# Optimization experiments

Measured on AMD Instinct MI355X. Metric: run time of the kernel, lower is better.

Reference implementation:

```python
import jax, jax.numpy as jnp
import numpy as np

N, B, E, H, Z, L = 8192, 256, 163840, 128, 256, 4
NFREQ = 10
EDGE_IN = 2 * H + 9 + 2 * NFREQ * 3  # 325


def _sin_emb(x):
    # SinusoidsEmbedding: x (E,3) -> (E, 2*NFREQ*3)
    freqs = 2 * jnp.pi * jnp.arange(NFREQ, dtype=x.dtype)
    e = (x[..., None] * freqs).reshape(x.shape[0], -1)  # (E, 3*NFREQ)
    return jnp.concatenate([jnp.sin(e), jnp.cos(e)], axis=-1)


def _seg_mean(x, idx, n):
    s = jax.ops.segment_sum(x, idx, num_segments=n)
    c = jax.ops.segment_sum(jnp.ones((x.shape[0], 1), x.dtype), idx, num_segments=n)
    return s / jnp.maximum(c, 1.0)  # empty segments -> 0, matching torch scatter-mean


def setup_inputs() -> dict:
    key = jax.random.key(0)
    ks = jax.random.split(key, 20)
    atom_types = jax.random.randint(ks[0], (N,), 0, 100)
    frac_coords = jax.random.uniform(ks[1], (N, 3), dtype=jnp.float32)
    lattices = jax.random.normal(ks[2], (B, 3, 3), dtype=jnp.float32)
    z = jax.random.normal(ks[3], (B, Z), dtype=jnp.float32)
    cemb = jax.random.uniform(ks[4], (B, 1), dtype=jnp.float32)
    edge_index = jax.random.randint(ks[5], (2, E), 0, N)
    node2graph = jnp.repeat(jnp.arange(B), N // B)  # 32 atoms per graph, sorted
    w = lambda k, *s: jax.random.normal(k, s, dtype=jnp.float32) * 0.05
    z0 = lambda *s: jnp.zeros(s, jnp.float32)
    return dict(
        atom_types=atom_types, frac_coords=frac_coords, lattices=lattices,
        z=z, cemb=cemb, edge_index=edge_index, node2graph=node2graph,
        emb_table=w(ks[6], 100, H),
        W_latent=w(ks[7], H + Z, H), b_latent=z0(H),
        edge_w1=w(ks[8], L, EDGE_IN, H), edge_b1=z0(L, H),
        edge_w2=w(ks[9], L, H, H), edge_b2=z0(L, H),
        node_w1=w(ks[10], L, 2 * H, H), node_b1=z0(L, H),
        node_w2=w(ks[11], L, H, H), node_b2=z0(L, H),
        mixin_w=w(ks[12], L, H, H),
        adapt_w1=w(ks[13], L, 1, H), adapt_b1=z0(L, H),
        adapt_w2=w(ks[14], L, H, H), adapt_b2=z0(L, H),
        W_coord=w(ks[15], H, 3),
        W_lattice=w(ks[16], H, 9),
    )


def _forward(frac_coords, lattices, z, cemb, emb_table, W_latent, b_latent,
             edge_w1, edge_b1, edge_w2, edge_b2, node_w1, node_b1, node_w2, node_b2,
             mixin_w, adapt_w1, adapt_b1, adapt_w2, adapt_b2, W_coord, W_lattice,
             atom_types, edge_index, node2graph):
    silu = jax.nn.silu
    src, dst = edge_index[0], edge_index[1]
    edge2graph = node2graph[src]
    # node embedding + latent conditioning
    h = emb_table[atom_types]  # (N,H)
    h = jnp.concatenate([h, z[node2graph]], axis=-1) @ W_latent + b_latent
    # per-edge geometric features (same across layers since frac_coords fixed)
    frac_diff = (frac_coords[dst] - frac_coords[src]) % 1.0  # (E,3)
    dis = _sin_emb(frac_diff)  # (E,60)
    # ip=True: lattice inner products, flattened per graph then gathered per edge
    lat_ips = jnp.einsum('bij,bkj->bik', lattices, lattices).reshape(B, 9)
    lat_e = lat_ips[edge2graph]  # (E,9)
    n = h.shape[0]
    for i in range(L):
        hi, hj = h[src], h[dst]
        einp = jnp.concatenate([hi, hj, dis, lat_e], axis=-1)  # (E,325)
        ef = silu(silu(einp @ edge_w1[i] + edge_b1[i]) @ edge_w2[i] + edge_b2[i])
        agg = _seg_mean(ef, src, n)  # scatter-mean back to src nodes
        nout = silu(silu(jnp.concatenate([h, agg], axis=-1) @ node_w1[i] + node_b1[i])
                    @ node_w2[i] + node_b2[i])
        h = h + nout  # residual
        # conditional-embedding adapter + mixin, broadcast per-graph to nodes
        c = silu(silu(cemb @ adapt_w1[i] + adapt_b1[i]) @ adapt_w2[i] + adapt_b2[i]) @ mixin_w[i]
        h = h + c[node2graph]
    coord_out = h @ W_coord  # (N,3), no bias
    graph_f = _seg_mean(h, node2graph, B)
    lattice_out = (graph_f @ W_lattice).reshape(B, 3, 3)
    lattice_out = jnp.einsum('bij,bjk->bik', lattice_out, lattices)  # ip=True
    return lattice_out, coord_out


def reference(atom_types, frac_coords, lattices, z, cemb, edge_index, node2graph,
              emb_table, W_latent, b_latent, edge_w1, edge_b1, edge_w2, edge_b2,
              node_w1, node_b1, node_w2, node_b2, mixin_w, adapt_w1, adapt_b1,
              adapt_w2, adapt_b2, W_coord, W_lattice):
    return _forward(frac_coords, lattices, z, cemb, emb_table, W_latent, b_latent,
                    edge_w1, edge_b1, edge_w2, edge_b2, node_w1, node_b1, node_w2,
                    node_b2, mixin_w, adapt_w1, adapt_b1, adapt_w2, adapt_b2,
                    W_coord, W_lattice, atom_types, edge_index, node2graph)
```

## Files before the change

### kernel.cpp

```cpp
#include <hip/hip_runtime.h>
#include <hip/hip_bf16.h>
#include <stdint.h>

#define NN 8192
#define BB 256
#define EE 163840
#define HH 128
#define ZZ 256
#define LL 4
#define TPB 5

typedef unsigned short u16;
typedef float  f32x4  __attribute__((ext_vector_type(4)));
typedef __bf16 bf16x8 __attribute__((ext_vector_type(8)));

__device__ __forceinline__ u16 f2bf(float f) {
  union { float f; uint32_t u; } v; v.f = f;
  uint32_t r = v.u + 0x7fffu + ((v.u >> 16) & 1u);
  return (u16)(r >> 16);
}
__device__ __forceinline__ float silu_f(float x) {
  return x * __builtin_amdgcn_rcpf(1.0f + __expf(-x));
}

// ... 18 lines not shown
    __syncthreads();
  }
  const int base = (t == 0) ? 0 : part[t - 1];
#pragma unroll
  for (int j = 0; j < 8; ++j) cursor[t * 8 + j] = base + v[j];
}

__global__ void k_scatter(const int* __restrict__ ei, int* __restrict__ cursor,
                          int* __restrict__ perm) {
  const int e = blockIdx.x * 256 + threadIdx.x;
  if (e < EE) {
    const int s = ei[e];
    const int ppos = atomicAdd(&cursor[s], 1);
    perm[ppos] = e;
  }
}

#define R_WT1S  (LL * 128 * 128)
#define R_WT1D  (LL * 128 * 128)
#define R_WT1G  (LL * 128 * 64)
#define R_WT2   (LL * 128 * 128)
#define R_NWT1  (LL * 128 * 256)
#define R_NWT2  (LL * 128 * 128)
#define R_HWT   (128 * 384)
#define R_EMB   (100 * 128)
#define R_Z     (BB * ZZ)
#define R_LIP   (BB * 9)
#define PREP_TOT (R_WT1S + R_WT1D + R_WT1G + R_WT2 + R_NWT1 + R_NWT2 + R_HWT + R_EMB + R_Z + R_LIP)

__global__ __launch_bounds__(256) void k_prep(
    const float* __restrict__ ew1, const float* __restrict__ ew2,
    const float* __restrict__ nw1, const float* __restrict__ nw2,
    const float* __restrict__ Wl,  const float* __restrict__ emb,
    const float* __restrict__ z,   const float* __restrict__ lat,
    u16* __restrict__ wt1s, u16* __restrict__ wt1d, u16* __restrict__ wt1g,
    u16* __restrict__ wt2,
    u16* __restrict__ nwt1, u16* __restrict__ nwt2,
    u16* __restrict__ hwt, u16* __restrict__ embbf, u16* __restrict__ zbf,
    float* __restrict__ lip) {
  int idx = blockIdx.x * 256 + threadIdx.x;
  if (idx < R_WT1S) {
    const int l = idx >> 14, rem = idx & 16383;
    const int n = rem >> 7, k = rem & 127;
    wt1s[idx] = f2bf(ew1[((size_t)l * 325 + k) * 128 + n]);
    return;
  }
  idx -= R_WT1S;
  if (idx < R_WT1D) {
    const int l = idx >> 14, rem = idx & 16383;
    const int n = rem >> 7, k = rem & 127;
    wt1d[idx] = f2bf(ew1[((size_t)l * 325 + 128 + k) * 128 + n]);
    return;
  }
  idx -= R_WT1D;
// ... 21 lines not shown
  if (idx < R_NWT2) {
    const int l = idx >> 14, rem = idx & 16383;
    const int n = rem >> 7, k = rem & 127;
    nwt2[idx] = f2bf(nw2[((size_t)l * 128 + k) * 128 + n]);
    return;
  }
  idx -= R_NWT2;
  if (idx < R_HWT) {
    const int n = idx / 384, k = idx % 384;
    hwt[idx] = f2bf(Wl[k * 128 + n]);
    return;
  }
  idx -= R_HWT;
  if (idx < R_EMB) { embbf[idx] = f2bf(emb[idx]); return; }
  idx -= R_EMB;
  if (idx < R_Z) { zbf[idx] = f2bf(z[idx]); return; }
  idx -= R_Z;
  if (idx < R_LIP) {
    const int b = idx / 9, j = idx % 9, i = j / 3, kk = j % 3;
    float s = 0.f;
#pragma unroll
    for (int mm = 0; mm < 3; ++mm) s += lat[b * 9 + i * 3 + mm] * lat[b * 9 + kk * 3 + mm];
    lip[b * 12 + j] = s;
  }
}

__global__ void k_gl(const float* __restrict__ ew1, const float* __restrict__ eb1,
                     const float* __restrict__ lip, float* __restrict__ Gl) {
  const int idx = blockIdx.x * 256 + threadIdx.x;
  if (idx >= LL * BB * 128) return;
  const int l = idx >> 15, rem = idx & 32767, g = rem >> 7, c = rem & 127;
  float s = eb1[l * 128 + c];
#pragma unroll
  for (int j = 0; j < 9; ++j)
    s += lip[g * 12 + j] * ew1[((size_t)l * 325 + 316 + j) * 128 + c];
  Gl[idx] = s;
}

__global__ __launch_bounds__(128) void k_adapt(
    const float* __restrict__ cemb, const float* __restrict__ aw1,
    const float* __restrict__ ab1, const float* __restrict__ aw2,
    const float* __restrict__ ab2, const float* __restrict__ mixin,
    float* __restrict__ call) {
  __shared__ float s1[128], s2[128];
  const int l = blockIdx.x >> 8, b = blockIdx.x & 255, c = threadIdx.x;
  const float ce = cemb[b];
  s1[c] = silu_f(ce * aw1[l * 128 + c] + ab1[l * 128 + c]);
  __syncthreads();
  float a = ab2[l * 128 + c];
  for (int k = 0; k < 128; ++k) a += s1[k] * aw2[(l * 128 + k) * 128 + c];
  s2[c] = silu_f(a);
  __syncthreads();
  float o = 0.f;
  for (int k = 0; k < 128; ++k) o += s2[k] * mixin[(l * 128 + k) * 128 + c];
  call[((size_t)l * 256 + b) * 128 + c] = o;
}

__global__ __launch_bounds__(256) void k_h0(
    const int* __restrict__ at, const int* __restrict__ n2g,
    const u16* __restrict__ embbf, const u16* __restrict__ zbf,
    const u16* __restrict__ hwt, const float* __restrict__ bl,
    float* __restrict__ h, u16* __restrict__ hbf) {
  __shared__ __align__(16) __bf16 einp[32][392];
  const int tid = threadIdx.x, lane = tid & 63, w = tid >> 6;
  const int lr = lane & 15, lk = (lane >> 4) * 8, rr = (lane >> 4) * 4;
  const int m = tid >> 3, p = tid & 7;
  const int n0 = blockIdx.x * 32;
  {
    const int n = n0 + m;
    const uint4* er = (const uint4*)(embbf + (size_t)at[n] * 128);
    *(uint4*)(&einp[m][p * 16])     = er[p * 2];
    *(uint4*)(&einp[m][p * 16 + 8]) = er[p * 2 + 1];
    const uint4* zr = (const uint4*)(zbf + (size_t)n2g[n] * 256);
#pragma unroll
    for (int q = 0; q < 4; ++q)
      *(uint4*)(&einp[m][128 + p * 32 + q * 8]) = zr[p * 4 + q];
  }
  __syncthreads();
  f32x4 acc[2][2] = {};
  const u16* w0 = hwt + (size_t)(w * 32 + lr) * 384 + lk;
  const u16* w1 = hwt + (size_t)(w * 32 + 16 + lr) * 384 + lk;
#pragma unroll
  for (int kb = 0; kb < 12; ++kb) {
    bf16x8 a0 = *(const bf16x8*)(&einp[lr][kb * 32 + lk]);
    bf16x8 a1 = *(const bf16x8*)(&einp[16 + lr][kb * 32 + lk]);
    bf16x8 b0 = *(const bf16x8*)(w0 + kb * 32);
    bf16x8 b1 = *(const bf16x8*)(w1 + kb * 32);
    acc[0][0] = __builtin_amdgcn_mfma_f32_16x16x32_bf16(a0, b0, acc[0][0], 0, 0, 0);
    acc[0][1] = __builtin_amdgcn_mfma_f32_16x16x32_bf16(a0, b1, acc[0][1], 0, 0, 0);
    acc[1][0] = __builtin_amdgcn_mfma_f32_16x16x32_bf16(a1, b0, acc[1][0], 0, 0, 0);
    acc[1][1] = __builtin_amdgcn_mfma_f32_16x16x32_bf16(a1, b1, acc[1][1], 0, 0, 0);
  }
#pragma unroll
  for (int mt = 0; mt < 2; ++mt)
#pragma unroll
    for (int nt = 0; nt < 2; ++nt) {
      const int col = w * 32 + nt * 16 + lr;
      const float bias = bl[col];
#pragma unroll
      for (int r = 0; r < 4; ++r) {
        const int n = n0 + mt * 16 + rr + r;
        const float s = acc[mt][nt][r] + bias;
        h[(size_t)n * 128 + col] = s;
        hbf[(size_t)n * 128 + col] = f2bf(s);
      }
    }
}

__global__ __launch_bounds__(256) void k_pnode(
    const u16* __restrict__ hbf, const u16* __restrict__ wt1s,
    const u16* __restrict__ wt1d, const float* __restrict__ Gl,
    const int* __restrict__ n2g, float* __restrict__ Ps, float* __restrict__ Pd) {
  __shared__ __align__(16) __bf16 hs[32][136];
  const int tid = threadIdx.x, lane = tid & 63, w = tid >> 6;
  const int lr = lane & 15, lk = (lane >> 4) * 8, rr = (lane >> 4) * 4;
  const int m = tid >> 3, p = tid & 7;
  const int n0 = blockIdx.x * 32;
  {
    const uint4* hr = (const uint4*)(hbf + (size_t)(n0 + m) * 128);
    *(uint4*)(&hs[m][p * 16])     = hr[p * 2];
    *(uint4*)(&hs[m][p * 16 + 8]) = hr[p * 2 + 1];
  }
  __syncthreads();
  f32x4 as[2][2] = {}, ad[2][2] = {};
  const u16* ws0 = wt1s + (size_t)(w * 32 + lr) * 128 + lk;
  const u16* ws1 = wt1s + (size_t)(w * 32 + 16 + lr) * 128 + lk;
  const u16* wd0 = wt1d + (size_t)(w * 32 + lr) * 128 + lk;
  const u16* wd1 = wt1d + (size_t)(w * 32 + 16 + lr) * 128 + lk;
#pragma unroll
  for (int kb = 0; kb < 4; ++kb) {
    bf16x8 a0 = *(const bf16x8*)(&hs[lr][kb * 32 + lk]);
    bf16x8 a1 = *(const bf16x8*)(&hs[16 + lr][kb * 32 + lk]);
    bf16x8 bs0 = *(const bf16x8*)(ws0 + kb * 32);
    bf16x8 bs1 = *(const bf16x8*)(ws1 + kb * 32);
    bf16x8 bd0 = *(const bf16x8*)(wd0 + kb * 32);
    bf16x8 bd1 = *(const bf16x8*)(wd1 + kb * 32);
    as[0][0] = __builtin_amdgcn_mfma_f32_16x16x32_bf16(a0, bs0, as[0][0], 0, 0, 0);
    as[0][1] = __builtin_amdgcn_mfma_f32_16x16x32_bf16(a0, bs1, as[0][1], 0, 0, 0);
    as[1][0] = __builtin_amdgcn_mfma_f32_16x16x32_bf16(a1, bs0, as[1][0], 0, 0, 0);
    as[1][1] = __builtin_amdgcn_mfma_f32_16x16x32_bf16(a1, bs1, as[1][1], 0, 0, 0);
    ad[0][0] = __builtin_amdgcn_mfma_f32_16x16x32_bf16(a0, bd0, ad[0][0], 0, 0, 0);
    ad[0][1] = __builtin_amdgcn_mfma_f32_16x16x32_bf16(a0, bd1, ad[0][1], 0, 0, 0);
    ad[1][0] = __builtin_amdgcn_mfma_f32_16x16x32_bf16(a1, bd0, ad[1][0], 0, 0, 0);
    ad[1][1] = __builtin_amdgcn_mfma_f32_16x16x32_bf16(a1, bd1, ad[1][1], 0, 0, 0);
  }
#pragma unroll
  for (int mt = 0; mt < 2; ++mt)
#pragma unroll
    for (int nt = 0; nt < 2; ++nt) {
      const int col = w * 32 + nt * 16 + lr;
#pragma unroll
      for (int r = 0; r < 4; ++r) {
        const int n = n0 + mt * 16 + rr + r;
        Ps[(size_t)n * 128 + col] = as[mt][nt][r] + Gl[(size_t)n2g[n] * 128 + col];
        Pd[(size_t)n * 128 + col] = ad[mt][nt][r];
      }
    }
}

__device__ __forceinline__ void write_sinemb(__bf16* rowp, int p, float f_d, float f_s) {
  float dd = f_d - f_s;
  dd -= floorf(dd);
  float s1, c1;
  __sincosf(dd * 6.2831853071795864769f, &s1, &c1);
  rowp[p * 10]      = (__bf16)0.0f;
  rowp[30 + p * 10] = (__bf16)1.0f;
  float sk = s1, ck = c1;
#pragma unroll
  for (int k = 1; k < 10; ++k) {
    rowp[p * 10 + k]      = (__bf16)sk;
    rowp[30 + p * 10 + k] = (__bf16)ck;
    const float sn = sk * c1 + ck * s1, cn = ck * c1 - sk * s1;
    sk = sn; ck = cn;
  }
}

__global__ __launch_bounds__(512, 2) void k_edge(
    const float* __restrict__ Ps, const float* __restrict__ Pd,
    const float* __restrict__ fc, const int* __restrict__ ei,
    const int* __restrict__ perm,
    const u16* __restrict__ wt1g, const u16* __restrict__ wt2,
    const float* __restrict__ eb2, float* __restrict__ agg) {
  __shared__ __align__(16) __bf16 eg[64][72];
  __shared__ __align__(16) __bf16 t1s[64][136];
  __shared__ int srcs[2][64], dsts[2][64];

  const int tid = threadIdx.x;
  const int lane = tid & 63, w = tid >> 6;
  const int wm = w >> 2, wn = w & 3;
  const int lr = lane & 15, lk = (lane >> 4) * 8, rr = (lane >> 4) * 4;
  const int m = tid >> 3, p = tid & 7;

  const u16* g0p  = wt1g + (size_t)(wn * 32 + lr) * 64 + lk;
  const u16* g1p  = wt1g + (size_t)(wn * 32 + 16 + lr) * 64 + lk;
  const u16* w2p0 = wt2 + (size_t)(wn * 32 + lr) * 128 + lk;
  const u16* w2p1 = wt2 + (size_t)(wn * 32 + 16 + lr) * 128 + lk;
  const float bias2_0 = eb2[wn * 32 + lr], bias2_1 = eb2[wn * 32 + 16 + lr];

  const int tile0 = blockIdx.x * TPB;

  for (int i = tid; i < 64 * 12; i += 512) eg[i / 12][60 + i % 12] = (__bf16)0.0f;

  {
    const int e = perm[tile0 * 64 + m];
    const int s = ei[e], d = ei[EE + e];
    if (p == 3) srcs[0][m] = s;
    if (p == 4) dsts[0][m] = d;
    if (p < 3) write_sinemb(&eg[m][0], p, fc[d * 3 + p], fc[s * 3 + p]);
  }
  __syncthreads();

  for (int t = 0; t < TPB; ++t) {
    const int cur = t & 1, nxt = cur ^ 1;
    const bool has_next = (t + 1 < TPB);
    int s_next = 0, d_next = 0;
    float f_d = 0.f, f_s = 0.f;
    if (has_next) {
      const int e = perm[(tile0 + t + 1) * 64 + m];
      s_next = ei[e]; d_next = ei[EE + e];
      if (p < 3) { f_d = fc[d_next * 3 + p]; f_s = fc[s_next * 3 + p]; }
    }

    {
      f32x4 acc[2][2];
#pragma unroll
      for (int mt = 0; mt < 2; ++mt)
#pragma unroll
        for (int r = 0; r < 4; ++r) {
          const int row = wm * 32 + mt * 16 + rr + r;
          const float* ps = Ps + (size_t)srcs[cur][row] * 128;
          const float* pd = Pd + (size_t)dsts[cur][row] * 128;
          const int c0 = wn * 32 + lr, c1 = wn * 32 + 16 + lr;
          acc[mt][0][r] = ps[c0] + pd[c0];
          acc[mt][1][r] = ps[c1] + pd[c1];
        }
      bf16x8 gb0[2], gb1[2];
      gb0[0] = *(const bf16x8*)(g0p);      gb0[1] = *(const bf16x8*)(g0p + 32);
      gb1[0] = *(const bf16x8*)(g1p);      gb1[1] = *(const bf16x8*)(g1p + 32);
#pragma unroll
      for (int kb = 0; kb < 2; ++kb) {
        bf16x8 a0 = *(const bf16x8*)(&eg[wm * 32 + lr][kb * 32 + lk]);
        bf16x8 a1 = *(const bf16x8*)(&eg[wm * 32 + 16 + lr][kb * 32 + lk]);
        acc[0][0] = __builtin_amdgcn_mfma_f32_16x16x32_bf16(a0, gb0[kb], acc[0][0], 0, 0, 0);
        acc[0][1] = __builtin_amdgcn_mfma_f32_16x16x32_bf16(a0, gb1[kb], acc[0][1], 0, 0, 0);
        acc[1][0] = __builtin_amdgcn_mfma_f32_16x16x32_bf16(a1, gb0[kb], acc[1][0], 0, 0, 0);
        acc[1][1] = __builtin_amdgcn_mfma_f32_16x16x32_bf16(a1, gb1[kb], acc[1][1], 0, 0, 0);
      }
      const int col0 = wn * 32 + lr, col1 = wn * 32 + 16 + lr;
#pragma unroll
      for (int mt = 0; mt < 2; ++mt)
#pragma unroll
        for (int r = 0; r < 4; ++r) {
          t1s[wm * 32 + mt * 16 + rr + r][col0] = (__bf16)silu_f(acc[mt][0][r]);
          t1s[wm * 32 + mt * 16 + rr + r][col1] = (__bf16)silu_f(acc[mt][1][r]);
        }
    }
    __syncthreads();

    if (has_next) {
      if (p == 3) srcs[nxt][m] = s_next;
      if (p == 4) dsts[nxt][m] = d_next;
      if (p < 3) write_sinemb(&eg[m][0], p, f_d, f_s);
    }
    f32x4 acc2[2][2] = {};
#pragma unroll
    for (int kb = 0; kb < 4; ++kb) {
      bf16x8 a0 = *(const bf16x8*)(&t1s[wm * 32 + lr][kb * 32 + lk]);
      bf16x8 a1 = *(const bf16x8*)(&t1s[wm * 32 + 16 + lr][kb * 32 + lk]);
      bf16x8 b0 = *(const bf16x8*)(w2p0 + kb * 32);
      bf16x8 b1 = *(const bf16x8*)(w2p1 + kb * 32);
      acc2[0][0] = __builtin_amdgcn_mfma_f32_16x16x32_bf16(a0, b0, acc2[0][0], 0, 0, 0);
      acc2[0][1] = __builtin_amdgcn_mfma_f32_16x16x32_bf16(a0, b1, acc2[0][1], 0, 0, 0);
      acc2[1][0] = __builtin_amdgcn_mfma_f32_16x16x32_bf16(a1, b0, acc2[1][0], 0, 0, 0);
      acc2[1][1] = __builtin_amdgcn_mfma_f32_16x16x32_bf16(a1, b1, acc2[1][1], 0, 0, 0);
    }
    __syncthreads();

    {
      const int col0 = wn * 32 + lr, col1 = wn * 32 + 16 + lr;
#pragma unroll
      for (int mt = 0; mt < 2; ++mt)
#pragma unroll
        for (int r = 0; r < 4; ++r) {
          t1s[wm * 32 + mt * 16 + rr + r][col0] = (__bf16)silu_f(acc2[mt][0][r] + bias2_0);
          t1s[wm * 32 + mt * 16 + rr + r][col1] = (__bf16)silu_f(acc2[mt][1][r] + bias2_1);
        }
    }
    __syncthreads();

    {
      const int col = tid & 127, seg = tid >> 7, r0 = seg * 16;
      const int* sr = srcs[cur];
      int curS = sr[r0];
      float a = 0.f;
#pragma unroll 4
      for (int r = 0; r < 16; ++r) {
        const int s = sr[r0 + r];
        if (s != curS) {
          unsafeAtomicAdd(&agg[(size_t)curS * HH + col], a);
          curS = s; a = 0.f;
        }
        a += (float)t1s[r0 + r][col];
      }
      unsafeAtomicAdd(&agg[(size_t)curS * HH + col], a);
    }
    __syncthreads();
  }
}

__global__ __launch_bounds__(256) void k_node(
    float* __restrict__ h, float* __restrict__ agg, const int* __restrict__ cnt,
    const u16* __restrict__ nwt1, const float* __restrict__ nb1,
    const u16* __restrict__ nwt2, const float* __restrict__ nb2,
    const float* __restrict__ cl, const int* __restrict__ n2g,
    u16* __restrict__ hbf) {
  __shared__ __align__(16) __bf16 einp[32][264];
  __shared__ __align__(16) __bf16 t1n[32][136];
  const int tid = threadIdx.x, lane = tid & 63, w = tid >> 6;
  const int lr = lane & 15, lk = (lane >> 4) * 8, rr = (lane >> 4) * 4;
  const int m = tid >> 3, p = tid & 7;
  const int n0 = blockIdx.x * 32;
  {
    const int n = n0 + m;
    const uint4* hr = (const uint4*)(hbf + (size_t)n * 128);
    *(uint4*)(&einp[m][p * 16])     = hr[p * 2];
    *(uint4*)(&einp[m][p * 16 + 8]) = hr[p * 2 + 1];
    const float inv = 1.f / fmaxf((float)cnt[n], 1.f);
    const float4* ar = (const float4*)(agg + (size_t)n * 128);
    union { __bf16 b[16]; uint4 u[2]; } tmp;
#pragma unroll
// ... 39 lines not shown
  {
    const u16* w0 = nwt2 + (size_t)(w * 32 + lr) * 128 + lk;
    const u16* w1 = nwt2 + (size_t)(w * 32 + 16 + lr) * 128 + lk;
#pragma unroll
    for (int kb = 0; kb < 4; ++kb) {
      bf16x8 a0 = *(const bf16x8*)(&t1n[lr][kb * 32 + lk]);
      bf16x8 a1 = *(const bf16x8*)(&t1n[16 + lr][kb * 32 + lk]);
      bf16x8 b0 = *(const bf16x8*)(w0 + kb * 32);
      bf16x8 b1 = *(const bf16x8*)(w1 + kb * 32);
      acc2[0][0] = __builtin_amdgcn_mfma_f32_16x16x32_bf16(a0, b0, acc2[0][0], 0, 0, 0);
      acc2[0][1] = __builtin_amdgcn_mfma_f32_16x16x32_bf16(a0, b1, acc2[0][1], 0, 0, 0);
      acc2[1][0] = __builtin_amdgcn_mfma_f32_16x16x32_bf16(a1, b0, acc2[1][0], 0, 0, 0);
      acc2[1][1] = __builtin_amdgcn_mfma_f32_16x16x32_bf16(a1, b1, acc2[1][1], 0, 0, 0);
    }
  }
#pragma unroll
  for (int mt = 0; mt < 2; ++mt)
#pragma unroll
    for (int nt = 0; nt < 2; ++nt) {
      const int col = w * 32 + nt * 16 + lr;
      const float bias = nb2[col];
#pragma unroll
      for (int r = 0; r < 4; ++r) {
        const int n = n0 + mt * 16 + rr + r;
        const float rv = h[(size_t)n * 128 + col] + silu_f(acc2[mt][nt][r] + bias)
                       + cl[(size_t)n2g[n] * 128 + col];
        h[(size_t)n * 128 + col] = rv;
        hbf[(size_t)n * 128 + col] = f2bf(rv);
        agg[(size_t)n * 128 + col] = 0.f;
      }
    }
}

__global__ __launch_bounds__(256) void k_coord(
    const float* __restrict__ h, const float* __restrict__ Wc, float* __restrict__ out) {
  const int idx = blockIdx.x * 256 + threadIdx.x;
  if (idx >= NN * 3) return;
  const int n = idx / 3, j = idx % 3;
  float s = 0.f;
  for (int k = 0; k < 128; ++k) s += h[n * 128 + k] * Wc[k * 3 + j];
  out[BB * 9 + idx] = s;
}

__global__ __launch_bounds__(128) void k_lattice(
    const float* __restrict__ h, const float* __restrict__ Wl9,
    const float* __restrict__ lat, float* __restrict__ out) {
  __shared__ float gf[128];
  __shared__ float lo[9];
  const int b = blockIdx.x, c = threadIdx.x;
  float s = 0.f;
  for (int mm = 0; mm < 32; ++mm) s += h[((size_t)b * 32 + mm) * 128 + c];
  gf[c] = s * (1.f / 32.f);
  __syncthreads();
  if (c < 9) {
    float t = 0.f;
    for (int k = 0; k < 128; ++k) t += gf[k] * Wl9[k * 9 + c];
    lo[c] = t;
  }
  __syncthreads();
  if (c < 9) {
    const int i = c / 3, kk = c % 3;
    float t = 0.f;
#pragma unroll
    for (int j = 0; j < 3; ++j) t += lo[i * 3 + j] * lat[b * 9 + j * 3 + kk];
    out[b * 9 + c] = t;
  }
}

extern "C" void kernel_launch(void* const* d_in, const int* in_sizes, int n_in,
                              void* d_out, int out_size, void* d_ws, size_t ws_size,
                              hipStream_t stream) {
  const int*   atom_types = (const int*)  d_in[0];
  const float* frac       = (const float*)d_in[1];
  const float* lattices   = (const float*)d_in[2];
  const float* z          = (const float*)d_in[3];
  const float* cemb       = (const float*)d_in[4];
  const int*   ei         = (const int*)  d_in[5];
  const int*   n2g        = (const int*)  d_in[6];
  const float* emb        = (const float*)d_in[7];
  const float* W_lat      = (const float*)d_in[8];
// ... 19 lines not shown
  size_t off = 0;
  auto carve = [&](size_t bytes) -> void* {
    void* r = base + off;
    off = (off + bytes + 255) & ~(size_t)255;
    return r;
  };
  float* h      = (float*)carve((size_t)NN * HH * 4);
  u16*   hbf    = (u16*)  carve((size_t)NN * HH * 2);
  float* agg    = (float*)carve((size_t)NN * HH * 4);
  float* Ps     = (float*)carve((size_t)NN * HH * 4);
  float* Pd     = (float*)carve((size_t)NN * HH * 4);
  float* Gl     = (float*)carve((size_t)LL * BB * HH * 4);
  int*   cnt    = (int*)  carve((size_t)NN * 4);
  int*   cursor = (int*)  carve((size_t)NN * 4);
  int*   perm   = (int*)  carve((size_t)EE * 4);
  float* lip    = (float*)carve((size_t)BB * 12 * 4);
  float* call   = (float*)carve((size_t)LL * BB * HH * 4);
  u16*   wt1s   = (u16*)  carve((size_t)R_WT1S * 2);
  u16*   wt1d   = (u16*)  carve((size_t)R_WT1D * 2);
  u16*   wt1g   = (u16*)  carve((size_t)R_WT1G * 2);
  u16*   wt2    = (u16*)  carve((size_t)R_WT2 * 2);
  u16*   nwt1   = (u16*)  carve((size_t)R_NWT1 * 2);
  u16*   nwt2   = (u16*)  carve((size_t)R_NWT2 * 2);
  u16*   hwt    = (u16*)  carve((size_t)R_HWT * 2);
  u16*   embbf  = (u16*)  carve((size_t)R_EMB * 2);
  u16*   zbf    = (u16*)  carve((size_t)R_Z * 2);

  hipMemsetAsync(cnt, 0, (size_t)NN * 4, stream);
  k_hist<<<EE / 256, 256, 0, stream>>>(ei, cnt);
  k_scan<<<1, 1024, 0, stream>>>(cnt, cursor);
  k_scatter<<<EE / 256, 256, 0, stream>>>(ei, cursor, perm);
  k_prep<<<(PREP_TOT + 255) / 256, 256, 0, stream>>>(
      ew1, ew2, nw1, nw2, W_lat, emb, z, lattices,
      wt1s, wt1d, wt1g, wt2, nwt1, nwt2, hwt, embbf, zbf, lip);
  k_gl<<<(LL * BB * 128 + 255) / 256, 256, 0, stream>>>(ew1, eb1, lip, Gl);
  k_adapt<<<LL * BB, 128, 0, stream>>>(cemb, aw1, ab1, aw2, ab2, mixin, call);
  k_h0<<<NN / 32, 256, 0, stream>>>(atom_types, n2g, embbf, zbf, hwt, b_lat, h, hbf);
  k_pnode<<<NN / 32, 256, 0, stream>>>(hbf, wt1s, wt1d, Gl, n2g, Ps, Pd);
  hipMemsetAsync(agg, 0, (size_t)NN * HH * 4, stream);

  for (int l = 0; l < LL; ++l) {
    k_edge<<<EE / (64 * TPB), 512, 0, stream>>>(Ps, Pd, frac, ei, perm,
        wt1g + (size_t)l * 128 * 64, wt2 + (size_t)l * 128 * 128,
        eb2 + l * 128, agg);
    k_node<<<NN / 32, 256, 0, stream>>>(h, agg, cnt,
        nwt1 + (size_t)l * 128 * 256, nb1 + l * 128,
        nwt2 + (size_t)l * 128 * 128, nb2 + l * 128,
        call + (size_t)l * BB * HH, n2g, hbf);
    if (l + 1 < LL)
      k_pnode<<<NN / 32, 256, 0, stream>>>(hbf,
          wt1s + (size_t)(l + 1) * 128 * 128, wt1d + (size_t)(l + 1) * 128 * 128,
          Gl + (size_t)(l + 1) * BB * HH, n2g, Ps, Pd);
  }

  k_coord<<<(NN * 3) / 256, 256, 0, stream>>>(h, Wc, out);
  k_lattice<<<BB, 128, 0, stream>>>(h, Wl9, lattices, out);
}
```

Baseline: 284.7 us.

## Precompute edge geometry once, fuse pnode into h0/node, merge output heads

```diff
diff --git a/kernel.cpp b/kernel.cpp
--- a/kernel.cpp
+++ b/kernel.cpp
@@ -56,6 +56,40 @@
     const int ppos = atomicAdd(&cursor[s], 1);
     perm[ppos] = e;
   }
+}
+
+__global__ __launch_bounds__(256) void k_geo(
+    const int* __restrict__ perm, const int* __restrict__ ei,
+    const float* __restrict__ fc,
+    int* __restrict__ sp, int* __restrict__ dp, u16* __restrict__ egp) {
+  const int i = blockIdx.x * 256 + threadIdx.x;
+  if (i >= EE) return;
+  const int e = perm[i];
+  const int s = ei[e], d = ei[EE + e];
+  sp[i] = s; dp[i] = d;
+  union { u16 b[64]; uint4 u[8]; } row;
+#pragma unroll
+  for (int p = 0; p < 3; ++p) {
+    float dd = fc[d * 3 + p] - fc[s * 3 + p];
+    dd -= floorf(dd);
+    float s1, c1;
+    __sincosf(dd * 6.2831853071795864769f, &s1, &c1);
+    row.b[p * 10]      = 0;
+    row.b[30 + p * 10] = f2bf(1.0f);
+    float sk = s1, ck = c1;
+#pragma unroll
+    for (int k = 1; k < 10; ++k) {
+      row.b[p * 10 + k]      = f2bf(sk);
+      row.b[30 + p * 10 + k] = f2bf(ck);
+      const float sn = sk * c1 + ck * s1, cn = ck * c1 - sk * s1;
+      sk = sn; ck = cn;
+    }
+  }
+#pragma unroll
+  for (int j = 60; j < 64; ++j) row.b[j] = 0;
+  uint4* out = (uint4*)(egp + (size_t)i * 64);
+#pragma unroll
+  for (int q = 0; q < 8; ++q) out[q] = row.u[q];
 }
 
 #define R_WT1S  (LL * 128 * 128)
@@ -67,19 +101,17 @@
 #define R_HWT   (128 * 384)
 #define R_EMB   (100 * 128)
 #define R_Z     (BB * ZZ)
-#define R_LIP   (BB * 9)
-#define PREP_TOT (R_WT1S + R_WT1D + R_WT1G + R_WT2 + R_NWT1 + R_NWT2 + R_HWT + R_EMB + R_Z + R_LIP)
+#define PREP_TOT (R_WT1S + R_WT1D + R_WT1G + R_WT2 + R_NWT1 + R_NWT2 + R_HWT + R_EMB + R_Z)
 
 __global__ __launch_bounds__(256) void k_prep(
     const float* __restrict__ ew1, const float* __restrict__ ew2,
     const float* __restrict__ nw1, const float* __restrict__ nw2,
     const float* __restrict__ Wl,  const float* __restrict__ emb,
-    const float* __restrict__ z,   const float* __restrict__ lat,
+    const float* __restrict__ z,
     u16* __restrict__ wt1s, u16* __restrict__ wt1d, u16* __restrict__ wt1g,
     u16* __restrict__ wt2,
     u16* __restrict__ nwt1, u16* __restrict__ nwt2,
-    u16* __restrict__ hwt, u16* __restrict__ embbf, u16* __restrict__ zbf,
-    float* __restrict__ lip) {
+    u16* __restrict__ hwt, u16* __restrict__ embbf, u16* __restrict__ zbf) {
   int idx = blockIdx.x * 256 + threadIdx.x;
   if (idx < R_WT1S) {
     const int l = idx >> 14, rem = idx & 16383;
@@ -131,26 +163,24 @@
   idx -= R_HWT;
   if (idx < R_EMB) { embbf[idx] = f2bf(emb[idx]); return; }
   idx -= R_EMB;
-  if (idx < R_Z) { zbf[idx] = f2bf(z[idx]); return; }
-  idx -= R_Z;
-  if (idx < R_LIP) {
-    const int b = idx / 9, j = idx % 9, i = j / 3, kk = j % 3;
-    float s = 0.f;
-#pragma unroll
-    for (int mm = 0; mm < 3; ++mm) s += lat[b * 9 + i * 3 + mm] * lat[b * 9 + kk * 3 + mm];
-    lip[b * 12 + j] = s;
-  }
+  if (idx < R_Z) { zbf[idx] = f2bf(z[idx]); }
 }
 
 __global__ void k_gl(const float* __restrict__ ew1, const float* __restrict__ eb1,
-                     const float* __restrict__ lip, float* __restrict__ Gl) {
+                     const float* __restrict__ lat, float* __restrict__ Gl) {
   const int idx = blockIdx.x * 256 + threadIdx.x;
   if (idx >= LL * BB * 128) return;
   const int l = idx >> 15, rem = idx & 32767, g = rem >> 7, c = rem & 127;
   float s = eb1[l * 128 + c];
 #pragma unroll
-  for (int j = 0; j < 9; ++j)
-    s += lip[g * 12 + j] * ew1[((size_t)l * 325 + 316 + j) * 128 + c];
+  for (int j = 0; j < 9; ++j) {
+    const int i = j / 3, kk = j % 3;
+    float lip = 0.f;
+#pragma unroll
+    for (int mm = 0; mm < 3; ++mm)
+      lip += lat[g * 9 + i * 3 + mm] * lat[g * 9 + kk * 3 + mm];
+    s += lip * ew1[((size_t)l * 325 + 316 + j) * 128 + c];
+  }
   Gl[idx] = s;
 }
 
@@ -177,8 +207,12 @@
     const int* __restrict__ at, const int* __restrict__ n2g,
     const u16* __restrict__ embbf, const u16* __restrict__ zbf,
     const u16* __restrict__ hwt, const float* __restrict__ bl,
-    float* __restrict__ h, u16* __restrict__ hbf) {
+    const u16* __restrict__ wt1s, const u16* __restrict__ wt1d,
+    const float* __restrict__ Gl,
+    float* __restrict__ h, u16* __restrict__ hbf,
+    float* __restrict__ Ps, float* __restrict__ Pd) {
   __shared__ __align__(16) __bf16 einp[32][392];
+  __bf16 (*hs)[136] = (__bf16(*)[136])&einp[0][0];
   const int tid = threadIdx.x, lane = tid & 63, w = tid >> 6;
   const int lr = lane & 15, lk = (lane >> 4) * 8, rr = (lane >> 4) * 4;
   const int m = tid >> 3, p = tid & 7;
@@ -195,19 +229,22 @@
   }
   __syncthreads();
   f32x4 acc[2][2] = {};
-  const u16* w0 = hwt + (size_t)(w * 32 + lr) * 384 + lk;
-  const u16* w1 = hwt + (size_t)(w * 32 + 16 + lr) * 384 + lk;
-#pragma unroll
-  for (int kb = 0; kb < 12; ++kb) {
-    bf16x8 a0 = *(const bf16x8*)(&einp[lr][kb * 32 + lk]);
-    bf16x8 a1 = *(const bf16x8*)(&einp[16 + lr][kb * 32 + lk]);
-    bf16x8 b0 = *(const bf16x8*)(w0 + kb * 32);
-    bf16x8 b1 = *(const bf16x8*)(w1 + kb * 32);
-    acc[0][0] = __builtin_amdgcn_mfma_f32_16x16x32_bf16(a0, b0, acc[0][0], 0, 0, 0);
-    acc[0][1] = __builtin_amdgcn_mfma_f32_16x16x32_bf16(a0, b1, acc[0][1], 0, 0, 0);
-    acc[1][0] = __builtin_amdgcn_mfma_f32_16x16x32_bf16(a1, b0, acc[1][0], 0, 0, 0);
-    acc[1][1] = __builtin_amdgcn_mfma_f32_16x16x32_bf16(a1, b1, acc[1][1], 0, 0, 0);
-  }
+  {
+    const u16* w0 = hwt + (size_t)(w * 32 + lr) * 384 + lk;
+    const u16* w1 = hwt + (size_t)(w * 32 + 16 + lr) * 384 + lk;
+#pragma unroll
+    for (int kb = 0; kb < 12; ++kb) {
+      bf16x8 a0 = *(const bf16x8*)(&einp[lr][kb * 32 + lk]);
+      bf16x8 a1 = *(const bf16x8*)(&einp[16 + lr][kb * 32 + lk]);
+      bf16x8 b0 = *(const bf16x8*)(w0 + kb * 32);
+      bf16x8 b1 = *(const bf16x8*)(w1 + kb * 32);
+      acc[0][0] = __builtin_amdgcn_mfma_f32_16x16x32_bf16(a0, b0, acc[0][0], 0, 0, 0);
+      acc[0][1] = __builtin_amdgcn_mfma_f32_16x16x32_bf16(a0, b1, acc[0][1], 0, 0, 0);
+      acc[1][0] = __builtin_amdgcn_mfma_f32_16x16x32_bf16(a1, b0, acc[1][0], 0, 0, 0);
+      acc[1][1] = __builtin_amdgcn_mfma_f32_16x16x32_bf16(a1, b1, acc[1][1], 0, 0, 0);
+    }
+  }
+  __syncthreads();
 #pragma unroll
   for (int mt = 0; mt < 2; ++mt)
 #pragma unroll
@@ -216,50 +253,38 @@
       const float bias = bl[col];
 #pragma unroll
       for (int r = 0; r < 4; ++r) {
-        const int n = n0 + mt * 16 + rr + r;
+        const int row = mt * 16 + rr + r;
         const float s = acc[mt][nt][r] + bias;
-        h[(size_t)n * 128 + col] = s;
-        hbf[(size_t)n * 128 + col] = f2bf(s);
+        h[(size_t)(n0 + row) * 128 + col] = s;
+        const u16 bf = f2bf(s);
+        hbf[(size_t)(n0 + row) * 128 + col] = bf;
+        hs[row][col] = *(const __bf16*)&bf;
       }
     }
-}
-
-__global__ __launch_bounds__(256) void k_pnode(
-    const u16* __restrict__ hbf, const u16* __restrict__ wt1s,
-    const u16* __restrict__ wt1d, const float* __restrict__ Gl,
-    const int* __restrict__ n2g, float* __restrict__ Ps, float* __restrict__ Pd) {
-  __shared__ __align__(16) __bf16 hs[32][136];
-  const int tid = threadIdx.x, lane = tid & 63, w = tid >> 6;
-  const int lr = lane & 15, lk = (lane >> 4) * 8, rr = (lane >> 4) * 4;
-  const int m = tid >> 3, p = tid & 7;
-  const int n0 = blockIdx.x * 32;
+  __syncthreads();
+  f32x4 as[2][2] = {}, ad[2][2] = {};
   {
-    const uint4* hr = (const uint4*)(hbf + (size_t)(n0 + m) * 128);
-    *(uint4*)(&hs[m][p * 16])     = hr[p * 2];
-    *(uint4*)(&hs[m][p * 16 + 8]) = hr[p * 2 + 1];
-  }
-  __syncthreads();
-  f32x4 as[2][2] = {}, ad[2][2] = {};
-  const u16* ws0 = wt1s + (size_t)(w * 32 + lr) * 128 + lk;
-  const u16* ws1 = wt1s + (size_t)(w * 32 + 16 + lr) * 128 + lk;
-  const u16* wd0 = wt1d + (size_t)(w * 32 + lr) * 128 + lk;
-  const u16* wd1 = wt1d + (size_t)(w * 32 + 16 + lr) * 128 + lk;
-#pragma unroll
-  for (int kb = 0; kb < 4; ++kb) {
-    bf16x8 a0 = *(const bf16x8*)(&hs[lr][kb * 32 + lk]);
-    bf16x8 a1 = *(const bf16x8*)(&hs[16 + lr][kb * 32 + lk]);
-    bf16x8 bs0 = *(const bf16x8*)(ws0 + kb * 32);
-    bf16x8 bs1 = *(const bf16x8*)(ws1 + kb * 32);
-    bf16x8 bd0 = *(const bf16x8*)(wd0 + kb * 32);
-    bf16x8 bd1 = *(const bf16x8*)(wd1 + kb * 32);
-    as[0][0] = __builtin_amdgcn_mfma_f32_16x16x32_bf16(a0, bs0, as[0][0], 0, 0, 0);
-    as[0][1] = __builtin_amdgcn_mfma_f32_16x16x32_bf16(a0, bs1, as[0][1], 0, 0, 0);
-    as[1][0] = __builtin_amdgcn_mfma_f32_16x16x32_bf16(a1, bs0, as[1][0], 0, 0, 0);
-    as[1][1] = __builtin_amdgcn_mfma_f32_16x16x32_bf16(a1, bs1, as[1][1], 0, 0, 0);
-    ad[0][0] = __builtin_amdgcn_mfma_f32_16x16x32_bf16(a0, bd0, ad[0][0], 0, 0, 0);
-    ad[0][1] = __builtin_amdgcn_mfma_f32_16x16x32_bf16(a0, bd1, ad[0][1], 0, 0, 0);
-    ad[1][0] = __builtin_amdgcn_mfma_f32_16x16x32_bf16(a1, bd0, ad[1][0], 0, 0, 0);
-    ad[1][1] = __builtin_amdgcn_mfma_f32_16x16x32_bf16(a1, bd1, ad[1][1], 0, 0, 0);
+    const u16* ws0 = wt1s + (size_t)(w * 32 + lr) * 128 + lk;
+    const u16* ws1 = wt1s + (size_t)(w * 32 + 16 + lr) * 128 + lk;
+    const u16* wd0 = wt1d + (size_t)(w * 32 + lr) * 128 + lk;
+    const u16* wd1 = wt1d + (size_t)(w * 32 + 16 + lr) * 128 + lk;
+#pragma unroll
+    for (int kb = 0; kb < 4; ++kb) {
+      bf16x8 a0 = *(const bf16x8*)(&hs[lr][kb * 32 + lk]);
+      bf16x8 a1 = *(const bf16x8*)(&hs[16 + lr][kb * 32 + lk]);
+      bf16x8 bs0 = *(const bf16x8*)(ws0 + kb * 32);
+      bf16x8 bs1 = *(const bf16x8*)(ws1 + kb * 32);
+      bf16x8 bd0 = *(const bf16x8*)(wd0 + kb * 32);
+      bf16x8 bd1 = *(const bf16x8*)(wd1 + kb * 32);
+      as[0][0] = __builtin_amdgcn_mfma_f32_16x16x32_bf16(a0, bs0, as[0][0], 0, 0, 0);
+      as[0][1] = __builtin_amdgcn_mfma_f32_16x16x32_bf16(a0, bs1, as[0][1], 0, 0, 0);
+      as[1][0] = __builtin_amdgcn_mfma_f32_16x16x32_bf16(a1, bs0, as[1][0], 0, 0, 0);
+      as[1][1] = __builtin_amdgcn_mfma_f32_16x16x32_bf16(a1, bs1, as[1][1], 0, 0, 0);
+      ad[0][0] = __builtin_amdgcn_mfma_f32_16x16x32_bf16(a0, bd0, ad[0][0], 0, 0, 0);
+      ad[0][1] = __builtin_amdgcn_mfma_f32_16x16x32_bf16(a0, bd1, ad[0][1], 0, 0, 0);
+      ad[1][0] = __builtin_amdgcn_mfma_f32_16x16x32_bf16(a1, bd0, ad[1][0], 0, 0, 0);
+      ad[1][1] = __builtin_amdgcn_mfma_f32_16x16x32_bf16(a1, bd1, ad[1][1], 0, 0, 0);
+    }
   }
 #pragma unroll
   for (int mt = 0; mt < 2; ++mt)
@@ -275,68 +300,31 @@
     }
 }
 
-__device__ __forceinline__ void write_sinemb(__bf16* rowp, int p, float f_d, float f_s) {
-  float dd = f_d - f_s;
-  dd -= floorf(dd);
-  float s1, c1;
-  __sincosf(dd * 6.2831853071795864769f, &s1, &c1);
-  rowp[p * 10]      = (__bf16)0.0f;
-  rowp[30 + p * 10] = (__bf16)1.0f;
-  float sk = s1, ck = c1;
-#pragma unroll
-  for (int k = 1; k < 10; ++k) {
-    rowp[p * 10 + k]      = (__bf16)sk;
-    rowp[30 + p * 10 + k] = (__bf16)ck;
-    const float sn = sk * c1 + ck * s1, cn = ck * c1 - sk * s1;
-    sk = sn; ck = cn;
-  }
-}
-
 __global__ __launch_bounds__(512, 2) void k_edge(
     const float* __restrict__ Ps, const float* __restrict__ Pd,
-    const float* __restrict__ fc, const int* __restrict__ ei,
-    const int* __restrict__ perm,
+    const int* __restrict__ sp, const int* __restrict__ dp,
+    const u16* __restrict__ egp,
     const u16* __restrict__ wt1g, const u16* __restrict__ wt2,
     const float* __restrict__ eb2, float* __restrict__ agg) {
-  __shared__ __align__(16) __bf16 eg[64][72];
-  __shared__ __align__(16) __bf16 t1s[64][136];
-  __shared__ int srcs[2][64], dsts[2][64];
+  __shared__ __align__(16) __bf16 buf0[64][136];
+  __shared__ __align__(16) __bf16 buf1[64][136];
 
   const int tid = threadIdx.x;
   const int lane = tid & 63, w = tid >> 6;
   const int wm = w >> 2, wn = w & 3;
   const int lr = lane & 15, lk = (lane >> 4) * 8, rr = (lane >> 4) * 4;
-  const int m = tid >> 3, p = tid & 7;
 
   const u16* g0p  = wt1g + (size_t)(wn * 32 + lr) * 64 + lk;
   const u16* g1p  = wt1g + (size_t)(wn * 32 + 16 + lr) * 64 + lk;
   const u16* w2p0 = wt2 + (size_t)(wn * 32 + lr) * 128 + lk;
   const u16* w2p1 = wt2 + (size_t)(wn * 32 + 16 + lr) * 128 + lk;
   const float bias2_0 = eb2[wn * 32 + lr], bias2_1 = eb2[wn * 32 + 16 + lr];
+  const int col0 = wn * 32 + lr, col1 = wn * 32 + 16 + lr;
 
   const int tile0 = blockIdx.x * TPB;
 
-  for (int i = tid; i < 64 * 12; i += 512) eg[i / 12][60 + i % 12] = (__bf16)0.0f;
-
-  {
-    const int e = perm[tile0 * 64 + m];
-    const int s = ei[e], d = ei[EE + e];
-    if (p == 3) srcs[0][m] = s;
-    if (p == 4) dsts[0][m] = d;
-    if (p < 3) write_sinemb(&eg[m][0], p, fc[d * 3 + p], fc[s * 3 + p]);
-  }
-  __syncthreads();
-
   for (int t = 0; t < TPB; ++t) {
-    const int cur = t & 1, nxt = cur ^ 1;
-    const bool has_next = (t + 1 < TPB);
-    int s_next = 0, d_next = 0;
-    float f_d = 0.f, f_s = 0.f;
-    if (has_next) {
-      const int e = perm[(tile0 + t + 1) * 64 + m];
-      s_next = ei[e]; d_next = ei[EE + e];
-      if (p < 3) { f_d = fc[d_next * 3 + p]; f_s = fc[s_next * 3 + p]; }
-    }
+    const int gi0 = (tile0 + t) * 64;
 
     {
       f32x4 acc[2][2];
@@ -345,83 +333,71 @@
 #pragma unroll
         for (int r = 0; r < 4; ++r) {
           const int row = wm * 32 + mt * 16 + rr + r;
-          const float* ps = Ps + (size_t)srcs[cur][row] * 128;
-          const float* pd = Pd + (size_t)dsts[cur][row] * 128;
-          const int c0 = wn * 32 + lr, c1 = wn * 32 + 16 + lr;
-          acc[mt][0][r] = ps[c0] + pd[c0];
-          acc[mt][1][r] = ps[c1] + pd[c1];
+          const float* ps = Ps + (size_t)sp[gi0 + row] * 128;
+          const float* pd = Pd + (size_t)dp[gi0 + row] * 128;
+          acc[mt][0][r] = ps[col0] + pd[col0];
+          acc[mt][1][r] = ps[col1] + pd[col1];
         }
       bf16x8 gb0[2], gb1[2];
       gb0[0] = *(const bf16x8*)(g0p);      gb0[1] = *(const bf16x8*)(g0p + 32);
       gb1[0] = *(const bf16x8*)(g1p);      gb1[1] = *(const bf16x8*)(g1p + 32);
 #pragma unroll
       for (int kb = 0; kb < 2; ++kb) {
-        bf16x8 a0 = *(const bf16x8*)(&eg[wm * 32 + lr][kb * 32 + lk]);
-        bf16x8 a1 = *(const bf16x8*)(&eg[wm * 32 + 16 + lr][kb * 32 + lk]);
+        bf16x8 a0 = *(const bf16x8*)(egp + (size_t)(gi0 + wm * 32 + lr) * 64 + kb * 32 + lk);
+        bf16x8 a1 = *(const bf16x8*)(egp + (size_t)(gi0 + wm * 32 + 16 + lr) * 64 + kb * 32 + lk);
         acc[0][0] = __builtin_amdgcn_mfma_f32_16x16x32_bf16(a0, gb0[kb], acc[0][0], 0, 0, 0);
         acc[0][1] = __builtin_amdgcn_mfma_f32_16x16x32_bf16(a0, gb1[kb], acc[0][1], 0, 0, 0);
         acc[1][0] = __builtin_amdgcn_mfma_f32_16x16x32_bf16(a1, gb0[kb], acc[1][0], 0, 0, 0);
         acc[1][1] = __builtin_amdgcn_mfma_f32_16x16x32_bf16(a1, gb1[kb], acc[1][1], 0, 0, 0);
       }
-      const int col0 = wn * 32 + lr, col1 = wn * 32 + 16 + lr;
 #pragma unroll
       for (int mt = 0; mt < 2; ++mt)
 #pragma unroll
         for (int r = 0; r < 4; ++r) {
-          t1s[wm * 32 + mt * 16 + rr + r][col0] = (__bf16)silu_f(acc[mt][0][r]);
-          t1s[wm * 32 + mt * 16 + rr + r][col1] = (__bf16)silu_f(acc[mt][1][r]);
+          buf0[wm * 32 + mt * 16 + rr + r][col0] = (__bf16)silu_f(acc[mt][0][r]);
+          buf0[wm * 32 + mt * 16 + rr + r][col1] = (__bf16)silu_f(acc[mt][1][r]);
         }
     }
     __syncthreads();
 
-    if (has_next) {
-      if (p == 3) srcs[nxt][m] = s_next;
-      if (p == 4) dsts[nxt][m] = d_next;
-      if (p < 3) write_sinemb(&eg[m][0], p, f_d, f_s);
-    }
-    f32x4 acc2[2][2] = {};
-#pragma unroll
-    for (int kb = 0; kb < 4; ++kb) {
-      bf16x8 a0 = *(const bf16x8*)(&t1s[wm * 32 + lr][kb * 32 + lk]);
-      bf16x8 a1 = *(const bf16x8*)(&t1s[wm * 32 + 16 + lr][kb * 32 + lk]);
-      bf16x8 b0 = *(const bf16x8*)(w2p0 + kb * 32);
-      bf16x8 b1 = *(const bf16x8*)(w2p1 + kb * 32);
-      acc2[0][0] = __builtin_amdgcn_mfma_f32_16x16x32_bf16(a0, b0, acc2[0][0], 0, 0, 0);
-      acc2[0][1] = __builtin_amdgcn_mfma_f32_16x16x32_bf16(a0, b1, acc2[0][1], 0, 0, 0);
-      acc2[1][0] = __builtin_amdgcn_mfma_f32_16x16x32_bf16(a1, b0, acc2[1][0], 0, 0, 0);
-      acc2[1][1] = __builtin_amdgcn_mfma_f32_16x16x32_bf16(a1, b1, acc2[1][1], 0, 0, 0);
-    }
-    __syncthreads();
-
     {
-      const int col0 = wn * 32 + lr, col1 = wn * 32 + 16 + lr;
+      f32x4 acc2[2][2] = {};
+#pragma unroll
+      for (int kb = 0; kb < 4; ++kb) {
+        bf16x8 a0 = *(const bf16x8*)(&buf0[wm * 32 + lr][kb * 32 + lk]);
+        bf16x8 a1 = *(const bf16x8*)(&buf0[wm * 32 + 16 + lr][kb * 32 + lk]);
+        bf16x8 b0 = *(const bf16x8*)(w2p0 + kb * 32);
+        bf16x8 b1 = *(const bf16x8*)(w2p1 + kb * 32);
+        acc2[0][0] = __builtin_amdgcn_mfma_f32_16x16x32_bf16(a0, b0, acc2[0][0], 0, 0, 0);
+        acc2[0][1] = __builtin_amdgcn_mfma_f32_16x16x32_bf16(a0, b1, acc2[0][1], 0, 0, 0);
+        acc2[1][0] = __builtin_amdgcn_mfma_f32_16x16x32_bf16(a1, b0, acc2[1][0], 0, 0, 0);
+        acc2[1][1] = __builtin_amdgcn_mfma_f32_16x16x32_bf16(a1, b1, acc2[1][1], 0, 0, 0);
+      }
 #pragma unroll
       for (int mt = 0; mt < 2; ++mt)
 #pragma unroll
         for (int r = 0; r < 4; ++r) {
-          t1s[wm * 32 + mt * 16 + rr + r][col0] = (__bf16)silu_f(acc2[mt][0][r] + bias2_0);
-          t1s[wm * 32 + mt * 16 + rr + r][col1] = (__bf16)silu_f(acc2[mt][1][r] + bias2_1);
+          buf1[wm * 32 + mt * 16 + rr + r][col0] = (__bf16)silu_f(acc2[mt][0][r] + bias2_0);
+          buf1[wm * 32 + mt * 16 + rr + r][col1] = (__bf16)silu_f(acc2[mt][1][r] + bias2_1);
         }
     }
     __syncthreads();
 
     {
       const int col = tid & 127, seg = tid >> 7, r0 = seg * 16;
-      const int* sr = srcs[cur];
-      int curS = sr[r0];
+      int curS = sp[gi0 + r0];
       float a = 0.f;
 #pragma unroll 4
       for (int r = 0; r < 16; ++r) {
-        const int s = sr[r0 + r];
+        const int s = sp[gi0 + r0 + r];
         if (s != curS) {
           unsafeAtomicAdd(&agg[(size_t)curS * HH + col], a);
           curS = s; a = 0.f;
         }
-        a += (float)t1s[r0 + r][col];
+        a += (float)buf1[r0 + r][col];
       }
       unsafeAtomicAdd(&agg[(size_t)curS * HH + col], a);
     }
-    __syncthreads();
   }
 }
 
@@ -430,7 +406,10 @@
     const u16* __restrict__ nwt1, const float* __restrict__ nb1,
     const u16* __restrict__ nwt2, const float* __restrict__ nb2,
     const float* __restrict__ cl, const int* __restrict__ n2g,
-    u16* __restrict__ hbf) {
+    u16* __restrict__ hbf,
+    const u16* __restrict__ wt1s, const u16* __restrict__ wt1d,
+    const float* __restrict__ Gl,
+    float* __restrict__ Ps, float* __restrict__ Pd) {
   __shared__ __align__(16) __bf16 einp[32][264];
   __shared__ __align__(16) __bf16 t1n[32][136];
   const int tid = threadIdx.x, lane = tid & 63, w = tid >> 6;
@@ -500,6 +479,7 @@
       acc2[1][1] = __builtin_amdgcn_mfma_f32_16x16x32_bf16(a1, b1, acc2[1][1], 0, 0, 0);
     }
   }
+  __syncthreads();
 #pragma unroll
   for (int mt = 0; mt < 2; ++mt)
 #pragma unroll
@@ -508,48 +488,94 @@
       const float bias = nb2[col];
 #pragma unroll
       for (int r = 0; r < 4; ++r) {
-        const int n = n0 + mt * 16 + rr + r;
+        const int row = mt * 16 + rr + r;
+        const int n = n0 + row;
         const float rv = h[(size_t)n * 128 + col] + silu_f(acc2[mt][nt][r] + bias)
                        + cl[(size_t)n2g[n] * 128 + col];
         h[(size_t)n * 128 + col] = rv;
-        hbf[(size_t)n * 128 + col] = f2bf(rv);
+        const u16 bf = f2bf(rv);
+        hbf[(size_t)n * 128 + col] = bf;
+        t1n[row][col] = *(const __bf16*)&bf;
         agg[(size_t)n * 128 + col] = 0.f;
       }
     }
-}
-
-__global__ __launch_bounds__(256) void k_coord(
-    const float* __restrict__ h, const float* __restrict__ Wc, float* __restrict__ out) {
-  const int idx = blockIdx.x * 256 + threadIdx.x;
-  if (idx >= NN * 3) return;
-  const int n = idx / 3, j = idx % 3;
-  float s = 0.f;
-  for (int k = 0; k < 128; ++k) s += h[n * 128 + k] * Wc[k * 3 + j];
-  out[BB * 9 + idx] = s;
-}
-
-__global__ __launch_bounds__(128) void k_lattice(
-    const float* __restrict__ h, const float* __restrict__ Wl9,
-    const float* __restrict__ lat, float* __restrict__ out) {
+  if (!wt1s) return;
+  __syncthreads();
+  f32x4 as[2][2] = {}, ad[2][2] = {};
+  {
+    const u16* ws0 = wt1s + (size_t)(w * 32 + lr) * 128 + lk;
+    const u16* ws1 = wt1s + (size_t)(w * 32 + 16 + lr) * 128 + lk;
+    const u16* wd0 = wt1d + (size_t)(w * 32 + lr) * 128 + lk;
+    const u16* wd1 = wt1d + (size_t)(w * 32 + 16 + lr) * 128 + lk;
+#pragma unroll
+    for (int kb = 0; kb < 4; ++kb) {
+      bf16x8 a0 = *(const bf16x8*)(&t1n[lr][kb * 32 + lk]);
+      bf16x8 a1 = *(const bf16x8*)(&t1n[16 + lr][kb * 32 + lk]);
+      bf16x8 bs0 = *(const bf16x8*)(ws0 + kb * 32);
+      bf16x8 bs1 = *(const bf16x8*)(ws1 + kb * 32);
+      bf16x8 bd0 = *(const bf16x8*)(wd0 + kb * 32);
+      bf16x8 bd1 = *(const bf16x8*)(wd1 + kb * 32);
+      as[0][0] = __builtin_amdgcn_mfma_f32_16x16x32_bf16(a0, bs0, as[0][0], 0, 0, 0);
+      as[0][1] = __builtin_amdgcn_mfma_f32_16x16x32_bf16(a0, bs1, as[0][1], 0, 0, 0);
+      as[1][0] = __builtin_amdgcn_mfma_f32_16x16x32_bf16(a1, bs0, as[1][0], 0, 0, 0);
+      as[1][1] = __builtin_amdgcn_mfma_f32_16x16x32_bf16(a1, bs1, as[1][1], 0, 0, 0);
+      ad[0][0] = __builtin_amdgcn_mfma_f32_16x16x32_bf16(a0, bd0, ad[0][0], 0, 0, 0);
+      ad[0][1] = __builtin_amdgcn_mfma_f32_16x16x32_bf16(a0, bd1, ad[0][1], 0, 0, 0);
+      ad[1][0] = __builtin_amdgcn_mfma_f32_16x16x32_bf16(a1, bd0, ad[1][0], 0, 0, 0);
+      ad[1][1] = __builtin_amdgcn_mfma_f32_16x16x32_bf16(a1, bd1, ad[1][1], 0, 0, 0);
+    }
+  }
+#pragma unroll
+  for (int mt = 0; mt < 2; ++mt)
+#pragma unroll
+    for (int nt = 0; nt < 2; ++nt) {
+      const int col = w * 32 + nt * 16 + lr;
+#pragma unroll
+      for (int r = 0; r < 4; ++r) {
+        const int n = n0 + mt * 16 + rr + r;
+        Ps[(size_t)n * 128 + col] = as[mt][nt][r] + Gl[(size_t)n2g[n] * 128 + col];
+        Pd[(size_t)n * 128 + col] = ad[mt][nt][r];
+      }
+    }
+}
+
+__global__ __launch_bounds__(256) void k_heads(
+    const float* __restrict__ h, const float* __restrict__ Wc,
+    const float* __restrict__ Wl9, const float* __restrict__ lat,
+    float* __restrict__ out) {
+  const int b = blockIdx.x, tid = threadIdx.x;
+  if (b < NN * 3 / 256) {
+    const int idx = b * 256 + tid;
+    const int n = idx / 3, j = idx % 3;
+    float s = 0.f;
+    for (int k = 0; k < 128; ++k) s += h[n * 128 + k] * Wc[k * 3 + j];
+    out[BB * 9 + idx] = s;
+    return;
+  }
+  const int g = b - NN * 3 / 256;
+  __shared__ float part[2][128];
   __shared__ float gf[128];
   __shared__ float lo[9];
-  const int b = blockIdx.x, c = threadIdx.x;
+  const int c = tid & 127, half = tid >> 7;
   float s = 0.f;
-  for (int mm = 0; mm < 32; ++mm) s += h[((size_t)b * 32 + mm) * 128 + c];
-  gf[c] = s * (1.f / 32.f);
-  __syncthreads();
-  if (c < 9) {
+  for (int mm = 0; mm < 16; ++mm)
+    s += h[((size_t)g * 32 + half * 16 + mm) * 128 + c];
+  part[half][c] = s;
+  __syncthreads();
+  if (tid < 128) gf[tid] = (part[0][tid] + part[1][tid]) * (1.f / 32.f);
+  __syncthreads();
+  if (tid < 9) {
     float t = 0.f;
-    for (int k = 0; k < 128; ++k) t += gf[k] * Wl9[k * 9 + c];
-    lo[c] = t;
-  }
-  __syncthreads();
-  if (c < 9) {
-    const int i = c / 3, kk = c % 3;
+    for (int k = 0; k < 128; ++k) t += gf[k] * Wl9[k * 9 + tid];
+    lo[tid] = t;
+  }
+  __syncthreads();
+  if (tid < 9) {
+    const int i = tid / 3, kk = tid % 3;
     float t = 0.f;
 #pragma unroll
-    for (int j = 0; j < 3; ++j) t += lo[i * 3 + j] * lat[b * 9 + j * 3 + kk];
-    out[b * 9 + c] = t;
+    for (int j = 0; j < 3; ++j) t += lo[i * 3 + j] * lat[g * 9 + j * 3 + kk];
+    out[g * 9 + tid] = t;
   }
 }
 
@@ -599,7 +625,9 @@
   int*   cnt    = (int*)  carve((size_t)NN * 4);
   int*   cursor = (int*)  carve((size_t)NN * 4);
   int*   perm   = (int*)  carve((size_t)EE * 4);
-  float* lip    = (float*)carve((size_t)BB * 12 * 4);
+  int*   sp     = (int*)  carve((size_t)EE * 4);
+  int*   dp     = (int*)  carve((size_t)EE * 4);
+  u16*   egp    = (u16*)  carve((size_t)EE * 64 * 2);
   float* call   = (float*)carve((size_t)LL * BB * HH * 4);
   u16*   wt1s   = (u16*)  carve((size_t)R_WT1S * 2);
   u16*   wt1d   = (u16*)  carve((size_t)R_WT1D * 2);
@@ -615,29 +643,30 @@
   k_hist<<<EE / 256, 256, 0, stream>>>(ei, cnt);
   k_scan<<<1, 1024, 0, stream>>>(cnt, cursor);
   k_scatter<<<EE / 256, 256, 0, stream>>>(ei, cursor, perm);
+  k_geo<<<EE / 256, 256, 0, stream>>>(perm, ei, frac, sp, dp, egp);
   k_prep<<<(PREP_TOT + 255) / 256, 256, 0, stream>>>(
-      ew1, ew2, nw1, nw2, W_lat, emb, z, lattices,
-      wt1s, wt1d, wt1g, wt2, nwt1, nwt2, hwt, embbf, zbf, lip);
-  k_gl<<<(LL * BB * 128 + 255) / 256, 256, 0, stream>>>(ew1, eb1, lip, Gl);
+      ew1, ew2, nw1, nw2, W_lat, emb, z,
+      wt1s, wt1d, wt1g, wt2, nwt1, nwt2, hwt, embbf, zbf);
+  k_gl<<<(LL * BB * 128 + 255) / 256, 256, 0, stream>>>(ew1, eb1, lattices, Gl);
   k_adapt<<<LL * BB, 128, 0, stream>>>(cemb, aw1, ab1, aw2, ab2, mixin, call);
-  k_h0<<<NN / 32, 256, 0, stream>>>(atom_types, n2g, embbf, zbf, hwt, b_lat, h, hbf);
-  k_pnode<<<NN / 32, 256, 0, stream>>>(hbf, wt1s, wt1d, Gl, n2g, Ps, Pd);
+  k_h0<<<NN / 32, 256, 0, stream>>>(atom_types, n2g, embbf, zbf, hwt, b_lat,
+                                    wt1s, wt1d, Gl, h, hbf, Ps, Pd);
   hipMemsetAsync(agg, 0, (size_t)NN * HH * 4, stream);
 
   for (int l = 0; l < LL; ++l) {
-    k_edge<<<EE / (64 * TPB), 512, 0, stream>>>(Ps, Pd, frac, ei, perm,
+    k_edge<<<EE / (64 * TPB), 512, 0, stream>>>(Ps, Pd, sp, dp, egp,
         wt1g + (size_t)l * 128 * 64, wt2 + (size_t)l * 128 * 128,
         eb2 + l * 128, agg);
+    const bool more = (l + 1 < LL);
     k_node<<<NN / 32, 256, 0, stream>>>(h, agg, cnt,
         nwt1 + (size_t)l * 128 * 256, nb1 + l * 128,
         nwt2 + (size_t)l * 128 * 128, nb2 + l * 128,
-        call + (size_t)l * BB * HH, n2g, hbf);
-    if (l + 1 < LL)
-      k_pnode<<<NN / 32, 256, 0, stream>>>(hbf,
-          wt1s + (size_t)(l + 1) * 128 * 128, wt1d + (size_t)(l + 1) * 128 * 128,
-          Gl + (size_t)(l + 1) * BB * HH, n2g, Ps, Pd);
-  }
-
-  k_coord<<<(NN * 3) / 256, 256, 0, stream>>>(h, Wc, out);
-  k_lattice<<<BB, 128, 0, stream>>>(h, Wl9, lattices, out);
-}
+        call + (size_t)l * BB * HH, n2g, hbf,
+        more ? wt1s + (size_t)(l + 1) * 128 * 128 : (const u16*)nullptr,
+        more ? wt1d + (size_t)(l + 1) * 128 * 128 : (const u16*)nullptr,
+        more ? Gl + (size_t)(l + 1) * BB * HH : (const float*)nullptr,
+        Ps, Pd);
+  }
+
+  k_heads<<<NN * 3 / 256 + BB, 256, 0, stream>>>(h, Wc, Wl9, lattices, out);
+}
```

Result: slower. 393.6 us (+38.3%).
